# Kernel optimization log

Measured on AMD Instinct MI355X. Metric: run time of the kernel, lower is better.

Reference implementation:

```python
import jax, jax.numpy as jnp
import numpy as np

D_E, D_ENC, D_DEC, H = 128, 256, 512, 8
HD = D_DEC // H
B, S, T, V, C = 32, 128, 128, 32000, 2


def gru_cell(x, h, Wih, Whh, bih, bhh):
    # PyTorch GRU cell: gates ordered (reset, update, new)
    gi = x @ Wih.T + bih
    gh = h @ Whh.T + bhh
    ir, iz, inn = jnp.split(gi, 3, axis=-1)
    hr, hz, hn = jnp.split(gh, 3, axis=-1)
    r = jax.nn.sigmoid(ir + hr)
    z = jax.nn.sigmoid(iz + hz)
    n = jnp.tanh(inn + r * hn)
    return (1.0 - z) * n + z * h


def setup_inputs():
    key = jax.random.key(0)
    ks = iter(jax.random.split(key, 40))
    def nrm(shape, s=0.05):
        return jax.random.normal(next(ks), shape, jnp.float32) * s
    inp = {}
    inp["nx"] = jax.random.randint(next(ks), (B, S), 0, V)
    inp["x"] = jax.random.randint(next(ks), (B, T), 0, V)
    inp["label"] = jax.random.randint(next(ks), (B,), 0, C)
    inp["tok_emb"] = nrm((V, D_E))
    inp["start_emb"] = nrm((1, D_E))
    inp["style_emb"] = nrm((C, D_DEC))
    for d in ("f", "b"):
        inp["enc_Wih_" + d] = nrm((3 * D_ENC, D_E))
        inp["enc_Whh_" + d] = nrm((3 * D_ENC, D_ENC))
        inp["enc_bih_" + d] = nrm((3 * D_ENC,))
        inp["enc_bhh_" + d] = nrm((3 * D_ENC,))
    inp["dec_Wih"] = nrm((3 * D_DEC, D_E))
    inp["dec_Whh"] = nrm((3 * D_DEC, D_DEC))
    inp["dec_bih"] = nrm((3 * D_DEC,))
    inp["dec_bhh"] = nrm((3 * D_DEC,))
    inp["attn_in_w"] = nrm((3 * D_DEC, D_DEC))
    inp["attn_in_b"] = nrm((3 * D_DEC,))
    inp["attn_out_w"] = nrm((D_DEC, D_DEC))
    inp["attn_out_b"] = nrm((D_DEC,))
    inp["ln_g"] = jnp.ones((D_DEC,), jnp.float32)
    inp["ln_b"] = jnp.zeros((D_DEC,), jnp.float32)
    inp["proj_w"] = nrm((V, D_DEC))
    inp["proj_b"] = nrm((V,))
    return inp


def _forward(nx, x, label, tok_emb, start_emb, style_emb,
             enc_Wih_f, enc_Whh_f, enc_bih_f, enc_bhh_f,
             enc_Wih_b, enc_Whh_b, enc_bih_b, enc_bhh_b,
             dec_Wih, dec_Whh, dec_bih, dec_bhh,
             attn_in_w, attn_in_b, attn_out_w, attn_out_b,
             ln_g, ln_b, proj_w, proj_b):
    b, s = nx.shape
    # --- bidirectional GRU encoder (dropout in eval mode => identity) ---
    emb = tok_emb[nx]                          # [B,S,dE]
    xs = jnp.swapaxes(emb, 0, 1)               # [S,B,dE]
    h0 = jnp.zeros((b, D_ENC), emb.dtype)

    def step_f(h, xt):
        h2 = gru_cell(xt, h, enc_Wih_f, enc_Whh_f, enc_bih_f, enc_bhh_f)
        return h2, h2

    def step_b(h, xt):
        h2 = gru_cell(xt, h, enc_Wih_b, enc_Whh_b, enc_bih_b, enc_bhh_b)
        return h2, h2

    _, out_f = jax.lax.scan(step_f, h0, xs)
    _, out_b = jax.lax.scan(step_b, h0, xs, reverse=True)
    memory = jnp.concatenate([out_f, out_b], axis=-1)   # [S,B,dDec] (seq-first, matches torch MHA)

    # --- precompute K/V projections of memory (invariant across decode steps) ---
    Wq, Wk, Wv = jnp.split(attn_in_w, 3, axis=0)
    bq, bk, bv = jnp.split(attn_in_b, 3)
    k = (memory @ Wk.T + bk).reshape(s, b, H, HD).transpose(1, 2, 0, 3)  # [B,H,S,HD]
    v = (memory @ Wv.T + bv).reshape(s, b, H, HD).transpose(1, 2, 0, 3)

    # --- teacher-forced decoder inputs: <start>, x[:,0], ..., x[:,T-2] ---
    dec_in = jnp.concatenate(
        [jnp.broadcast_to(start_emb[None, :, :], (b, 1, D_E)), tok_emb[x[:, :-1]]], axis=1)
    dec_xs = jnp.swapaxes(dec_in, 0, 1)        # [T,B,dE]
    h_init = style_emb[label]                  # [B,dDec]
    scale = 1.0 / np.sqrt(HD).astype(np.float32)

    def dec_step(h, xt):
        h_dec = gru_cell(xt, h, dec_Wih, dec_Whh, dec_bih, dec_bhh)      # [B,dDec]
        q = (h_dec @ Wq.T + bq).reshape(b, H, HD)
        scores = jnp.einsum('bhd,bhsd->bhs', q, k) * scale
        attn = jax.nn.softmax(scores, axis=-1)
        ctx = jnp.einsum('bhs,bhsd->bhd', attn, v).reshape(b, D_DEC)
        c = ctx @ attn_out_w.T + attn_out_b
        y = h_dec + c
        mu = jnp.mean(y, axis=-1, keepdims=True)
        var = jnp.var(y, axis=-1, keepdims=True)
        h_new = (y - mu) / jnp.sqrt(var + 1e-5) * ln_g + ln_b            # LayerNorm
        logits = h_new @ proj_w.T + proj_b                               # [B,V]
        return h_new, logits

    _, logits = jax.lax.scan(dec_step, h_init, dec_xs)   # [T,B,V]
    return jnp.swapaxes(logits, 0, 1)                    # [B,T,V]


def reference(nx, x, label, tok_emb, start_emb, style_emb,
              enc_Wih_f, enc_Whh_f, enc_bih_f, enc_bhh_f,
              enc_Wih_b, enc_Whh_b, enc_bih_b, enc_bhh_b,
              dec_Wih, dec_Whh, dec_bih, dec_bhh,
              attn_in_w, attn_in_b, attn_out_w, attn_out_b,
              ln_g, ln_b, proj_w, proj_b):
    return _forward(nx, x, label, tok_emb, start_emb, style_emb,
                    enc_Wih_f, enc_Whh_f, enc_bih_f, enc_bhh_f,
                    enc_Wih_b, enc_Whh_b, enc_bih_b, enc_bhh_b,
                    dec_Wih, dec_Whh, dec_bih, dec_bhh,
                    attn_in_w, attn_in_b, attn_out_w, attn_out_b,
                    ln_g, ln_b, proj_w, proj_b)
```

## Files before the change

### kernel.cpp

```cpp
#include <hip/hip_runtime.h>
#include <math.h>

typedef float f4 __attribute__((ext_vector_type(4)));
typedef short short8 __attribute__((ext_vector_type(8)));
typedef unsigned short us4 __attribute__((ext_vector_type(4)));

#define DEV static __device__ __forceinline__
#define AGENT __HIP_MEMORY_SCOPE_AGENT

DEV float bf2f(unsigned short u){ unsigned int x=((unsigned int)u)<<16; float f; __builtin_memcpy(&f,&x,4); return f; }
DEV unsigned short f2bf(float f){ unsigned int x; __builtin_memcpy(&x,&f,4); return (unsigned short)((x + 0x7fffu + ((x>>16)&1u))>>16); }

struct bfpair { short hi, lo; };
DEV bfpair splitbf(float v){
  bfpair p;
  unsigned short h_ = f2bf(v);
  p.hi = (short)h_;
  p.lo = (short)f2bf(v - bf2f(h_));
  return p;
}

DEV unsigned long long ldA64(const void* p){
  return __hip_atomic_load((const unsigned long long*)p, __ATOMIC_RELAXED, AGENT);
}
DEV void f2of(unsigned long long q, float* f0, float* f1){
  unsigned int lo=(unsigned int)q, hi=(unsigned int)(q>>32);
  __builtin_memcpy(f0,&lo,4); __builtin_memcpy(f1,&hi,4);
}

DEV void ld1x16_sc(const void* p, f4* o){
  asm volatile(
    "global_load_dwordx4 %0, %1, off sc0 sc1\n\t"
    "s_waitcnt vmcnt(0)"
    : "=&v"(o[0]) : "v"(p) : "memory");
}
DEV void ld8x16_sc(const void* p, f4* o){
  asm volatile(
    "global_load_dwordx4 %0, %8, off sc0 sc1\n\t"
    "global_load_dwordx4 %1, %8, off offset:16 sc0 sc1\n\t"
    "global_load_dwordx4 %2, %8, off offset:32 sc0 sc1\n\t"
    "global_load_dwordx4 %3, %8, off offset:48 sc0 sc1\n\t"
    "global_load_dwordx4 %4, %8, off offset:64 sc0 sc1\n\t"
    "global_load_dwordx4 %5, %8, off offset:80 sc0 sc1\n\t"
    "global_load_dwordx4 %6, %8, off offset:96 sc0 sc1\n\t"
    "global_load_dwordx4 %7, %8, off offset:112 sc0 sc1\n\t"
    "s_waitcnt vmcnt(0)"
    : "=&v"(o[0]),"=&v"(o[1]),"=&v"(o[2]),"=&v"(o[3]),
      "=&v"(o[4]),"=&v"(o[5]),"=&v"(o[6]),"=&v"(o[7])
    : "v"(p) : "memory");
}
DEV void ld16x16_sc(const void* p, f4* o){
  asm volatile(
    "global_load_dwordx4 %0, %16, off sc0 sc1\n\t"
    "global_load_dwordx4 %1, %16, off offset:16 sc0 sc1\n\t"
    "global_load_dwordx4 %2, %16, off offset:32 sc0 sc1\n\t"
    "global_load_dwordx4 %3, %16, off offset:48 sc0 sc1\n\t"
    "global_load_dwordx4 %4, %16, off offset:64 sc0 sc1\n\t"
    "global_load_dwordx4 %5, %16, off offset:80 sc0 sc1\n\t"
    "global_load_dwordx4 %6, %16, off offset:96 sc0 sc1\n\t"
    "global_load_dwordx4 %7, %16, off offset:112 sc0 sc1\n\t"
    "global_load_dwordx4 %8, %16, off offset:128 sc0 sc1\n\t"
    "global_load_dwordx4 %9, %16, off offset:144 sc0 sc1\n\t"
    "global_load_dwordx4 %10, %16, off offset:160 sc0 sc1\n\t"
    "global_load_dwordx4 %11, %16, off offset:176 sc0 sc1\n\t"
    "global_load_dwordx4 %12, %16, off offset:192 sc0 sc1\n\t"
    "global_load_dwordx4 %13, %16, off offset:208 sc0 sc1\n\t"
    "global_load_dwordx4 %14, %16, off offset:224 sc0 sc1\n\t"
    "global_load_dwordx4 %15, %16, off offset:240 sc0 sc1\n\t"
    "s_waitcnt vmcnt(0)"
    : "=&v"(o[0]),"=&v"(o[1]),"=&v"(o[2]),"=&v"(o[3]),
      "=&v"(o[4]),"=&v"(o[5]),"=&v"(o[6]),"=&v"(o[7]),
      "=&v"(o[8]),"=&v"(o[9]),"=&v"(o[10]),"=&v"(o[11]),
      "=&v"(o[12]),"=&v"(o[13]),"=&v"(o[14]),"=&v"(o[15])
    : "v"(p) : "memory");
}
DEV void st8x16_sc(void* p, const f4* v){
  asm volatile(
    "global_store_dwordx4 %8, %0, off sc0 sc1\n\t"
    "global_store_dwordx4 %8, %1, off offset:16 sc0 sc1\n\t"
    "global_store_dwordx4 %8, %2, off offset:32 sc0 sc1\n\t"
    "global_store_dwordx4 %8, %3, off offset:48 sc0 sc1\n\t"
    "global_store_dwordx4 %8, %4, off offset:64 sc0 sc1\n\t"
    "global_store_dwordx4 %8, %5, off offset:80 sc0 sc1\n\t"
    "global_store_dwordx4 %8, %6, off offset:96 sc0 sc1\n\t"
    "global_store_dwordx4 %8, %7, off offset:112 sc0 sc1\n\t"
    "s_waitcnt vmcnt(0)"
    :: "v"(v[0]),"v"(v[1]),"v"(v[2]),"v"(v[3]),
       "v"(v[4]),"v"(v[5]),"v"(v[6]),"v"(v[7]),"v"(p) : "memory");
}

DEV int lds_off(int row,int strideShorts,int kShort){
  return row*strideShorts*2 + ((((kShort & ~7)*2) ^ ((row & 7)<<4)) + (kShort & 7)*2);
}
DEV void st8(unsigned short* lds,int row,int strideShorts,int k0,short8 v){
  *(short8*)((char*)lds + lds_off(row,strideShorts,k0)) = v;
}
DEV short8 ldfrag(const unsigned short* lds,int rowBase,int strideShorts,int k0){
  int lane = (int)(threadIdx.x & 63u);
  int row = rowBase + (lane & 15);
  int k = k0 + (lane >> 4)*8;
  return *(const short8*)((const char*)lds + lds_off(row,strideShorts,k));
}

DEV float dot8(f4 a0, f4 a1, short8 w){
  return a0[0]*bf2f((unsigned short)w[0]) + a0[1]*bf2f((unsigned short)w[1])
       + a0[2]*bf2f((unsigned short)w[2]) + a0[3]*bf2f((unsigned short)w[3])
       + a1[0]*bf2f((unsigned short)w[4]) + a1[1]*bf2f((unsigned short)w[5])
       + a1[2]*bf2f((unsigned short)w[6]) + a1[3]*bf2f((unsigned short)w[7]);
}

DEV void gbar_slot(int* slot, int nwg){
  __syncthreads();
  if (threadIdx.x==0){
    __hip_atomic_fetch_add(slot,1,__ATOMIC_RELAXED,AGENT);
    while (__hip_atomic_load(slot,__ATOMIC_RELAXED,AGENT) < nwg){
      __builtin_amdgcn_s_sleep(2);
    }
  }
  __syncthreads();
}

DEV void dbar(int* ctrs, int wg, int target){
  __syncthreads();
  if (threadIdx.x < 64){
    if (threadIdx.x == 0)
      __hip_atomic_store(&ctrs[wg*32], target, __ATOMIC_RELAXED, AGENT);
    for(;;){
      int v = __hip_atomic_load(&ctrs[(int)threadIdx.x*32], __ATOMIC_RELAXED, AGENT);
      if (__all(v >= target)) break;
      __builtin_amdgcn_s_sleep(2);
    }
  }
  __syncthreads();
}
DEV void vwait(int* ctrs, int target){
  if (threadIdx.x < 64){
    for(;;){
      int v = __hip_atomic_load(&ctrs[(int)threadIdx.x*32], __ATOMIC_RELAXED, AGENT);
      if (__all(v >= target)) break;
      __builtin_amdgcn_s_sleep(64);
    }
  }
  __syncthreads();
}
DEV void cwait(int* cctrs, int target){
  if (threadIdx.x < 64){
    for(;;){
      int v = __hip_atomic_load(&cctrs[((int)threadIdx.x & 7)*32], __ATOMIC_RELAXED, AGENT);
      if (__all(v >= target)) break;
      __builtin_amdgcn_s_sleep(64);
    }
  }
  __syncthreads();
}

__global__ void cvt_kernel(const float* __restrict__ src, unsigned short* __restrict__ dst, int n4){
  int stride = gridDim.x*blockDim.x;
  for (long i = blockIdx.x*blockDim.x + threadIdx.x; i < n4; i += stride){
    f4 v = *(const f4*)(src + i*4);
    us4 o; o[0]=f2bf(v[0]); o[1]=f2bf(v[1]); o[2]=f2bf(v[2]); o[3]=f2bf(v[3]);
    *(us4*)(dst + i*4) = o;
  }
}

__global__ void embed_kernel(const int* __restrict__ nx, const int* __restrict__ x,
  const int* __restrict__ label, const float* __restrict__ tok,
  const float* __restrict__ start, const float* __restrict__ style,
  unsigned short* __restrict__ embE, unsigned short* __restrict__ embD,
  float* __restrict__ h0)
{
  const int half = 4096*32;
  int i = blockIdx.x*256 + threadIdx.x;
  if (i < 2*half){
    const bool dec = i >= half;
    int j = dec ? i - half : i;
    int m = j >> 5, c4 = j & 31;
    int b = m & 31, tt = m >> 5;
    const float* src;
    if (!dec) src = tok + (long)nx[b*128 + tt]*128;
    else src = (tt == 0) ? start : (tok + (long)x[b*128 + tt - 1]*128);
    f4 v = *(const f4*)(src + c4*4);
    us4 o; o[0]=f2bf(v[0]); o[1]=f2bf(v[1]); o[2]=f2bf(v[2]); o[3]=f2bf(v[3]);
    *(us4*)((dec ? embD : embE) + (long)m*128 + c4*4) = o;
  } else {
    int j = i - 2*half;
    if (j < 4096){
      int b = j >> 7, c4 = j & 127;
      *(f4*)(h0 + b*512 + c4*4) = *(const f4*)(style + (long)label[b]*512 + c4*4);
    }
  }
}

__global__ void kv_reshape(const float* __restrict__ kvp, unsigned short* __restrict__ Kb, unsigned short* __restrict__ Vb){
  long i = (long)blockIdx.x*256 + threadIdx.x;
  if (i >= (long)4096*1024) return;
  int m = (int)(i >> 10), n = (int)(i & 1023);
  int s = m >> 5, b = m & 31;
  unsigned short bv = f2bf(kvp[i]);
  if (n < 512){
    int hh = n >> 6, d = n & 63;
    Kb[((long)(b*8 + hh)*128 + s)*64 + d] = bv;
  } else {
    int n2 = n - 512; int hh = n2 >> 6, d = n2 & 63;
    Vb[((long)(b*8 + hh)*64 + d)*128 + s] = bv;
  }
}

template<int MODE>
__global__ __launch_bounds__(256,2) void gemm64(
  const unsigned short* __restrict__ Bw, const float* __restrict__ bias,
  float* __restrict__ C, int M, int N, int K, int ldC,
  const unsigned short* __restrict__ Abf,
  const float* __restrict__ Af0, const float* __restrict__ Af1)
{
  __shared__ unsigned short a_s[64*64];
  __shared__ unsigned short b_s[64*64];
  const int tid = threadIdx.x, lane = tid & 63, wv = tid >> 6;
  const long mb = (long)blockIdx.x*64, nb = (long)blockIdx.y*64;
  f4 z = {0.f,0.f,0.f,0.f};
  f4 acc[4] = {z,z,z,z};
  const int r = tid >> 2, q = tid & 3, k0 = q*16;
  for (int kb = 0; kb < K; kb += 64){
    if (MODE==0){
      const unsigned short* src = Abf + (mb + r)*K + kb + k0;
      st8(a_s, r, 64, k0,   *(const short8*)src);
      st8(a_s, r, 64, k0+8, *(const short8*)(src+8));
    } else {
      float tmp[16];
      long m = mb + r;
      int kg = kb + k0;
      const float* base = (kg < 256) ? (Af0 + m*256 + kg) : (Af1 + m*256 + (kg - 256));
      #pragma unroll
      for (int i=0;i<16;i++) tmp[i] = base[i];
      short8 v0, v1;
      #pragma unroll
      for (int i=0;i<8;i++){ v0[i] = (short)f2bf(tmp[i]); v1[i] = (short)f2bf(tmp[8+i]); }
      st8(a_s, r, 64, k0, v0); st8(a_s, r, 64, k0+8, v1);
    }
    {
      const unsigned short* src = Bw + (nb + r)*K + kb + k0;
      st8(b_s, r, 64, k0,   *(const short8*)src);
      st8(b_s, r, 64, k0+8, *(const short8*)(src+8));
    }
    __syncthreads();
    #pragma unroll
    for (int kf=0; kf<2; kf++){
      short8 bfr = ldfrag(b_s, wv*16, 64, kf*32);
      #pragma unroll
      for (int mt=0; mt<4; mt++){
        short8 afr = ldfrag(a_s, mt*16, 64, kf*32);
        acc[mt] = __builtin_amdgcn_mfma_f32_16x16x32_bf16(afr, bfr, acc[mt], 0,0,0);
      }
    }
    __syncthreads();
  }
  const long col = nb + wv*16 + (lane & 15);
  const float bs = bias[col];
  #pragma unroll
  for (int mt=0; mt<4; mt++){
    #pragma unroll
    for (int rr=0; rr<4; rr++){
      long row = mb + mt*16 + (lane>>4)*4 + rr;
      C[row*(long)ldC + col] = acc[mt][rr] + bs;
    }
  }
}

__global__ __launch_bounds__(384) void enc_kernel(
  const float* __restrict__ WhhF_f, const float* __restrict__ WhhB_f,
  const float* __restrict__ GIF, const float* __restrict__ GIB,
  const float* __restrict__ bhhF, const float* __restrict__ bhhB,
  float* __restrict__ OUTF, float* __restrict__ OUTB,
  float* __restrict__ Hf,
  int* bar)
{
  __shared__ unsigned short whh_hi[96*256];
  __shared__ unsigned short whh_lo[96*256];
  __shared__ unsigned short a_hi[32*256];
  __shared__ unsigned short a_lo[32*256];
  __shared__ float ghscr[32*96];
  const int tid = threadIdx.x;
  const int wg = blockIdx.x;
  const int dir = wg >> 3, wgl = wg & 7;
  const float* Whh_f = dir ? WhhB_f : WhhF_f;
  const float* GI = dir ? GIB : GIF;
  const float* bhh = dir ? bhhB : bhhF;
  float* OUT = dir ? OUTB : OUTF;

  for (int idx = tid; idx < 96*32; idx += 384){
    int lr = idx >> 5, ch = idx & 31;
    int g_ = lr >> 5, jj = lr & 31;
    const float* wsrc = Whh_f + (long)(g_*256 + wgl*32 + jj)*256 + ch*8;
    short8 vh, vl;
    #pragma unroll
    for (int i=0;i<8;i++){ bfpair p = splitbf(wsrc[i]); vh[i] = p.hi; vl[i] = p.lo; }
    st8(whh_hi, lr, 256, ch*8, vh);
    st8(whh_lo, lr, 256, ch*8, vl);
  }
  __syncthreads();
  for (int t = 0; t < 128; t++){
    const int s = dir ? (127 - t) : t;
    const float* hbr = Hf + ((size_t)((t&1)*2 + dir))*(32*256);
    float* hbw = Hf + ((size_t)(((t+1)&1)*2 + dir))*(32*256);
    if (tid < 256){
      int b = tid >> 3, kg = tid & 7;
      const unsigned long long* hs = (const unsigned long long*)(hbr + b*256 + kg*32);
      #pragma unroll
      for (int c=0;c<4;c++){
        short8 vh, vl;
        #pragma unroll
        for (int i2=0;i2<4;i2++){
          unsigned long long qv = ldA64(hs + c*4 + i2);
          float f0, f1; f2of(qv, &f0, &f1);
          bfpair p0 = splitbf(f0), p1 = splitbf(f1);
          vh[i2*2] = p0.hi; vl[i2*2] = p0.lo;
          vh[i2*2+1] = p1.hi; vl[i2*2+1] = p1.lo;
        }
        st8(a_hi, b, 256, kg*32 + c*8, vh);
        st8(a_lo, b, 256, kg*32 + c*8, vl);
      }
    }
    __syncthreads();
    {
      const int wv = tid >> 6;
      f4 acc0 = {0.f,0.f,0.f,0.f}, acc1 = {0.f,0.f,0.f,0.f};
      #pragma unroll
      for (int kf=0; kf<8; kf++){
        short8 bhi = ldfrag(whh_hi, wv*16, 256, kf*32);
        short8 blo = ldfrag(whh_lo, wv*16, 256, kf*32);
        short8 ah0 = ldfrag(a_hi, 0, 256, kf*32);
        short8 al0 = ldfrag(a_lo, 0, 256, kf*32);
        short8 ah1 = ldfrag(a_hi, 16, 256, kf*32);
        short8 al1 = ldfrag(a_lo, 16, 256, kf*32);
        acc0 = __builtin_amdgcn_mfma_f32_16x16x32_bf16(ah0, bhi, acc0, 0,0,0);
        acc0 = __builtin_amdgcn_mfma_f32_16x16x32_bf16(al0, bhi, acc0, 0,0,0);
        acc0 = __builtin_amdgcn_mfma_f32_16x16x32_bf16(ah0, blo, acc0, 0,0,0);
        acc1 = __builtin_amdgcn_mfma_f32_16x16x32_bf16(ah1, bhi, acc1, 0,0,0);
        acc1 = __builtin_amdgcn_mfma_f32_16x16x32_bf16(al1, bhi, acc1, 0,0,0);
        acc1 = __builtin_amdgcn_mfma_f32_16x16x32_bf16(ah1, blo, acc1, 0,0,0);
      }
      const int lane = tid & 63;
      const int cl = wv*16 + (lane & 15);
      #pragma unroll
      for (int rr=0; rr<4; rr++){
        int r0 = (lane>>4)*4 + rr;
        ghscr[r0*96 + cl] = acc0[rr];
        ghscr[(16+r0)*96 + cl] = acc1[rr];
      }
    }
    __syncthreads();
    for (int task = tid; task < 1024; task += 384){
      int b = task >> 5, jj = task & 31;
      int jg = wgl*32 + jj;
      float ghr = ghscr[b*96 + jj]      + bhh[jg];
      float ghz = ghscr[b*96 + 32 + jj] + bhh[256 + jg];
      float ghn = ghscr[b*96 + 64 + jj] + bhh[512 + jg];
      const float* gi = GI + ((long)s*32 + b)*768;
      float r_ = 1.f/(1.f + __expf(-(gi[jg] + ghr)));
      float z_ = 1.f/(1.f + __expf(-(gi[256+jg] + ghz)));
      float n_ = tanhf(gi[512+jg] + r_*ghn);
      float hp = __hip_atomic_load(&hbr[b*256 + jg], __ATOMIC_RELAXED, AGENT);
      float hn = (1.f - z_)*n_ + z_*hp;
      OUT[((long)s*32 + b)*256 + jg] = hn;
      __hip_atomic_store(&hbw[b*256 + jg], hn, __ATOMIC_RELAXED, AGENT);
    }
    gbar_slot(bar + dir*128 + t, 8);
  }
}

struct DecS {
  unsigned short whh_hi[32*512];
  unsigned short whh_lo[32*512];
  unsigned short a_hi[32*512];
  unsigned short a_lo[32*512];
  float scr[32*64];
  float attn_l[4*128];
  float ctxs[4*64];
  float redm[32*8*2];
  float murs[64];
  float hnfr[32*8];
  float lngl[512], lnbl[512];
  float s1l[24], s2l[24];
};
struct VocS {
  unsigned short a_s[128*512];
  unsigned short b_s[64*64];
  float gl[512];
  float s2g[176];
};
struct CvtS {
  float redm[32*8*2];
  float murs[64];
};
union SU { DecS d; VocS v; CvtS c; };

__global__ __launch_bounds__(256,1) void dec_fused(
  const float* __restrict__ Whh_f,
  const unsigned short* __restrict__ WqBf,
  const unsigned short* __restrict__ Wout,
  const unsigned short* __restrict__ Kbf,
  const unsigned short* __restrict__ Vbf,
  const float* __restrict__ GI,
  const float* __restrict__ bhh,
  const float* __restrict__ aib,
  const float* __restrict__ aob,
  const float* __restrict__ lng,
  const float* __restrict__ lnb,
  const float* __restrict__ h0,
  float* __restrict__ Y,
  unsigned int* __restrict__ hdec32,
  unsigned short* __restrict__ Ybf,
  const unsigned short* __restrict__ Pbf,
  const float* __restrict__ projWf,
  const float* __restrict__ projB,
  float* __restrict__ out,
  int* ctrs)
{
  __shared__ SU s;
  const int tid = threadIdx.x;
  const int lane = tid & 63, wv = tid >> 6;
  int* cctrs = ctrs + 2048;

  if (blockIdx.x < 64){
    const int wg = blockIdx.x;
    const int h = wg >> 3, bg = wg & 7;
    const int jbase = wg*8;
    const int cw = wg & 7;

    if (tid < 24){ s.d.s1l[tid] = 0.f; s.d.s2l[tid] = 0.f; }
    __syncthreads();
    for (int idx = tid; idx < 32*64; idx += 256){
      int lr = idx >> 6, ch = idx & 63;
      short8 vh = {0,0,0,0,0,0,0,0}, vl = {0,0,0,0,0,0,0,0};
      if (lr < 24){
        int g_ = lr >> 3, jj = lr & 7;
        const float* wsrc = Whh_f + (long)(g_*512 + jbase + jj)*512 + ch*8;
        float s1p = 0.f, s2p = 0.f;
        #pragma unroll
        for (int i=0;i<8;i++){
          float wvv = wsrc[i];
          float gv = lng[ch*8+i];
          float bv = lnb[ch*8+i];
          float wp = wvv*gv;
          bfpair p = splitbf(wp);
          vh[i] = p.hi; vl[i] = p.lo;
          s1p += wp; s2p += bv*wvv;
        }
        atomicAdd(&s.d.s1l[lr], s1p);
        atomicAdd(&s.d.s2l[lr], s2p);
      }
      st8(s.d.whh_hi, lr, 512, ch*8, vh);
      st8(s.d.whh_lo, lr, 512, ch*8, vl);
    }
    for (int i = tid; i < 512; i += 256){ s.d.lngl[i] = lng[i]; s.d.lnbl[i] = lnb[i]; }

    const int qrow = h*64 + wv*16 + (lane & 15);
    const int kb0q = (lane>>4)*8;
    const unsigned short* wqbase = WqBf + (long)qrow*512 + kb0q;
    const int b_l = wv;
    const int bglob = bg*4 + b_l;
    const unsigned short* kbase = Kbf + ((long)(bglob*8 + h)*128 + lane*2)*64;
    const unsigned short* vbase = Vbf + ((long)(bglob*8 + h)*64 + lane)*128;
    const int jp = tid & 127;
    const unsigned short* wobase = Wout + (long)(jp*4)*512 + h*64;
    const float qb = aib[h*64 + wv*16 + (lane & 15)];
    const int bA = tid >> 3, kgA = tid & 7;
    const int jjA = tid & 7;
    const int jgA = jbase + jjA;
    const float bhr = bhh[jgA], bhz = bhh[512 + jgA], bhn = bhh[1024 + jgA];
    const float aobv = aob[jgA];
    __syncthreads();

    int lgen = 0;
    float gir = GI[((long)0*32 + bA)*1536 + jgA];
    float giz = GI[((long)0*32 + bA)*1536 + 512 + jgA];
    float gin = GI[((long)0*32 + bA)*1536 + 1024 + jgA];
    for (int t = 0; t < 128; t++){
      if (t == 0){
        const float* src = h0 + bA*512 + kgA*64;
        #pragma unroll
        for (int c=0;c<8;c++){
          short8 vh, vl;
          #pragma unroll
          for (int i=0;i<8;i++){
            float v = src[c*8+i];
            float gv = s.d.lngl[kgA*64 + c*8 + i];
            bfpair p = splitbf(v/gv);
            vh[i] = p.hi; vl[i] = p.lo;
            if (kgA == h && c == cw) s.d.hnfr[bA*8+i] = v;
          }
          st8(s.d.a_hi, bA, 512, kgA*64 + c*8, vh);
          st8(s.d.a_lo, bA, 512, kgA*64 + c*8, vl);
        }
        __syncthreads();
      } else {
        f4 yv[16];
        ld16x16_sc(Y + ((long)(t-1)*32 + bA)*512 + kgA*64, yv);
        float sm = 0.f, sq = 0.f;
        #pragma unroll
        for (int c=0;c<8;c++){
          short8 vh, vl;
          #pragma unroll
          for (int e=0;e<8;e++){
            float f = yv[c*2 + (e>>2)][e&3];
            sm += f; sq += f*f;
            bfpair p = splitbf(f);
            vh[e] = p.hi; vl[e] = p.lo;
            if (kgA == h && c == cw) s.d.hnfr[bA*8+e] = f;
          }
          st8(s.d.a_hi, bA, 512, kgA*64 + c*8, vh);
          st8(s.d.a_lo, bA, 512, kgA*64 + c*8, vl);
        }
        s.d.redm[(bA*8+kgA)*2] = sm; s.d.redm[(bA*8+kgA)*2+1] = sq;
        __syncthreads();
        if (tid < 32){
          float S1=0.f, S2=0.f;
          #pragma unroll
          for (int i=0;i<8;i++){ S1 += s.d.redm[(tid*8+i)*2]; S2 += s.d.redm[(tid*8+i)*2+1]; }
          float mu = S1*(1.f/512.f);
          float var = S2*(1.f/512.f) - mu*mu;
          s.d.murs[tid*2] = mu; s.d.murs[tid*2+1] = rsqrtf(var + 1e-5f);
        }
        __syncthreads();
      }
      {
        const int mt = wv >> 1, nt = wv & 1;
        f4 acc = {0.f,0.f,0.f,0.f};
        #pragma unroll
        for (int kf=0; kf<16; kf++){
          short8 bhi = ldfrag(s.d.whh_hi, nt*16, 512, kf*32);
          short8 blo = ldfrag(s.d.whh_lo, nt*16, 512, kf*32);
          short8 ahi = ldfrag(s.d.a_hi, mt*16, 512, kf*32);
          short8 alo = ldfrag(s.d.a_lo, mt*16, 512, kf*32);
          acc = __builtin_amdgcn_mfma_f32_16x16x32_bf16(ahi, bhi, acc, 0,0,0);
          acc = __builtin_amdgcn_mfma_f32_16x16x32_bf16(alo, bhi, acc, 0,0,0);
          acc = __builtin_amdgcn_mfma_f32_16x16x32_bf16(ahi, blo, acc, 0,0,0);
        }
        const int cl = nt*16 + (lane & 15);
        if (cl < 24){
          #pragma unroll
          for (int rr=0; rr<4; rr++){
            int row = mt*16 + (lane>>4)*4 + rr;
            s.d.scr[row*32 + cl] = acc[rr];
          }
        }
      }
      __syncthreads();
      {
        const float mu = t ? s.d.murs[bA*2] : 0.f;
        const float rsv = t ? s.d.murs[bA*2+1] : 1.f;
        const float c2 = rsv*mu;
        float ghr = rsv*s.d.scr[bA*32 + jjA]      - c2*s.d.s1l[jjA]      + (t ? s.d.s2l[jjA]      : 0.f) + bhr;
        float ghz = rsv*s.d.scr[bA*32 + 8 + jjA]  - c2*s.d.s1l[8 + jjA]  + (t ? s.d.s2l[8 + jjA]  : 0.f) + bhz;
        float ghn = rsv*s.d.scr[bA*32 + 16 + jjA] - c2*s.d.s1l[16 + jjA] + (t ? s.d.s2l[16 + jjA] : 0.f) + bhn;
        float r_ = 1.f/(1.f + __expf(-(gir + ghr)));
        float z_ = 1.f/(1.f + __expf(-(giz + ghz)));
        float n_ = tanhf(gin + r_*ghn);
        float hpv = s.d.hnfr[bA*8 + jjA];
        float hp = t ? (hpv - mu)*rsv*s.d.lngl[jgA] + s.d.lnbl[jgA] : hpv;
        float hd = (1.f - z_)*n_ + z_*hp;
        unsigned int hb = (unsigned int)f2bf(hd);
        unsigned int other = (unsigned int)__shfl_xor((int)hb, 1);
        if ((jjA & 1) == 0){
          unsigned int pack = hb | (other << 16);
          __hip_atomic_store(&hdec32[bA*256 + (jgA >> 1)], pack, __ATOMIC_RELAXED, AGENT);
        }
        __hip_atomic_store(&Y[((long)t*32 + bA)*512 + jgA], hd + aobv, __ATOMIC_RELAXED, AGENT);
      }
      dbar(ctrs, wg, ++lgen);
      {
        const int r4 = tid >> 6, ch = tid & 63;
        f4 hv;
        ld1x16_sc(hdec32 + (bg*4 + r4)*256 + ch*4, &hv);
        short8 v;
        #pragma unroll
        for (int w2=0; w2<4; w2++){
          float fv = hv[w2];
          unsigned int u; __builtin_memcpy(&u, &fv, 4);
          v[w2*2]   = (short)(u & 0xffff);
          v[w2*2+1] = (short)(u >> 16);
        }
        st8(s.d.a_hi, r4, 512, ch*8, v);
      }
      __syncthreads();
      {
        f4 acc0 = {0.f,0.f,0.f,0.f};
        #pragma unroll
        for (int kf=0; kf<16; kf++){
          short8 bfr = *(const short8*)(wqbase + kf*32);
          acc0 = __builtin_amdgcn_mfma_f32_16x16x32_bf16(ldfrag(s.d.a_hi, 0, 512, kf*32), bfr, acc0, 0,0,0);
        }
        const int cl = wv*16 + (lane & 15);
        if ((lane >> 4) == 0){
          #pragma unroll
          for (int rr=0; rr<4; rr++)
            s.d.scr[rr*64 + cl] = acc0[rr] + qb;
        }
      }
      __syncthreads();
      {
        const f4* qp = (const f4*)(s.d.scr + b_l*64);
        float s0 = 0.f, s1 = 0.f;
        #pragma unroll
        for (int c=0;c<8;c++) s0 += dot8(qp[c*2], qp[c*2+1], *(const short8*)(kbase + c*8));
        #pragma unroll
        for (int c=0;c<8;c++) s1 += dot8(qp[c*2], qp[c*2+1], *(const short8*)(kbase + 64 + c*8));
        s0 *= 0.125f; s1 *= 0.125f;
        float mx = fmaxf(s0, s1);
        #pragma unroll
        for (int o=1;o<64;o<<=1) mx = fmaxf(mx, __shfl_xor(mx, o));
        float e0 = __expf(s0 - mx), e1 = __expf(s1 - mx);
        float sm = e0 + e1;
        #pragma unroll
        for (int o=1;o<64;o<<=1) sm += __shfl_xor(sm, o);
        float inv = 1.f/sm;
        s.d.attn_l[b_l*128 + lane*2]   = e0*inv;
        s.d.attn_l[b_l*128 + lane*2+1] = e1*inv;
      }
      __syncthreads();
      {
        const f4* ap = (const f4*)(s.d.attn_l + b_l*128);
        float cx = 0.f;
        #pragma unroll
        for (int c=0;c<16;c++) cx += dot8(ap[c*2], ap[c*2+1], *(const short8*)(vbase + c*8));
        s.d.ctxs[b_l*64 + lane] = cx;
      }
      __syncthreads();
      {
        const int b2 = tid >> 7;
        #pragma unroll
        for (int jj=0;jj<4;jj++){
          const unsigned short* wb = wobase + (long)jj*512;
          short8 w0 = *(const short8*)(wb);
          short8 w1 = *(const short8*)(wb+8);
          short8 w2 = *(const short8*)(wb+16);
          short8 w3 = *(const short8*)(wb+24);
          short8 w4 = *(const short8*)(wb+32);
          short8 w5 = *(const short8*)(wb+40);
          short8 w6 = *(const short8*)(wb+48);
          short8 w7 = *(const short8*)(wb+56);
          #pragma unroll
          for (int bb=0; bb<2; bb++){
            const int bl = b2 + bb*2;
            const int bgl = bg*4 + bl;
            const f4* cp = (const f4*)(s.d.ctxs + bl*64);
            float cj = dot8(cp[0], cp[1], w0) + dot8(cp[2], cp[3], w1)
                     + dot8(cp[4], cp[5], w2) + dot8(cp[6], cp[7], w3)
                     + dot8(cp[8], cp[9], w4) + dot8(cp[10], cp[11], w5)
                     + dot8(cp[12], cp[13], w6) + dot8(cp[14], cp[15], w7);
            atomicAdd(&Y[((long)t*32 + bgl)*512 + jp*4 + jj], cj);
          }
        }
      }
      if (t < 127){
        long base = ((long)(t+1)*32 + bA)*1536 + jgA;
        gir = GI[base];
        giz = GI[base + 512];
        gin = GI[base + 1024];
      }
      dbar(ctrs, wg, ++lgen);
    }
  } else if (blockIdx.x < 72){
    const int w = blockIdx.x - 64;
    const int rr = tid >> 3, seg = tid & 7;
    for (int c = 0; c < 16; c++){
      vwait(ctrs, 16*(c+1));
      long m = (long)c*256 + w*32 + rr;
      f4 yv[16];
      ld16x16_sc(Y + m*512 + seg*64, yv);
      float sm = 0.f, sq = 0.f;
      #pragma unroll
      for (int i=0;i<16;i++){
        f4 v = yv[i];
        sm += v[0]+v[1]+v[2]+v[3];
        sq += v[0]*v[0]+v[1]*v[1]+v[2]*v[2]+v[3]*v[3];
      }
      s.c.redm[(rr*8+seg)*2] = sm; s.c.redm[(rr*8+seg)*2+1] = sq;
      __syncthreads();
      if (tid < 32){
        float S1=0.f, S2=0.f;
        #pragma unroll
        for (int i=0;i<8;i++){ S1 += s.c.redm[(tid*8+i)*2]; S2 += s.c.redm[(tid*8+i)*2+1]; }
        float mu = S1*(1.f/512.f);
        float var = S2*(1.f/512.f) - mu*mu;
        s.c.murs[tid*2] = mu; s.c.murs[tid*2+1] = rsqrtf(var + 1e-5f);
      }
      __syncthreads();
      const float mu = s.c.murs[rr*2], rsv = s.c.murs[rr*2+1];
      f4 ob[8];
      #pragma unroll
      for (int i2=0;i2<32;i2++){
        float a0 = (yv[(2*i2)>>2][(2*i2)&3] - mu)*rsv;
        float a1v = (yv[(2*i2+1)>>2][(2*i2+1)&3] - mu)*rsv;
        unsigned int u = (unsigned int)f2bf(a0) | ((unsigned int)f2bf(a1v)<<16);
        float uf; __builtin_memcpy(&uf,&u,4);
        ob[i2>>2][i2&3] = uf;
      }
      st8x16_sc(Ybf + m*512 + seg*64, ob);
      __syncthreads();
      if (tid == 0)
        __hip_atomic_store(&cctrs[w*32], c+1, __ATOMIC_RELAXED, AGENT);
    }
  } else {
    const int w2 = blockIdx.x - 72;
    const int c0 = w2*174;
    const int cn = (32000 - c0 < 174) ? (32000 - c0) : 174;
    for (int cc = tid; cc < 176; cc += 256){
      if (cc < cn){
        const float* pw = projWf + (long)(c0+cc)*512;
        float s2 = 0.f;
        for (int k=0;k<512;k++) s2 += lnb[k]*pw[k];
        s.v.s2g[cc] = s2;
      }
    }
    for (int i = tid; i < 512; i += 256) s.v.gl[i] = lng[i];
    __syncthreads();
    const f4 z4 = {0.f,0.f,0.f,0.f};
    for (int c=0; c<16; c++){
      cwait(cctrs, c+1);
      for (int half=0; half<2; half++){
        const long rbase = (long)c*256 + half*128;
        {
          const int row = tid >> 1, seg = tid & 1;
          const unsigned short* src = Ybf + (rbase + row)*512 + seg*256;
          #pragma unroll
          for (int blk=0; blk<2; blk++){
            f4 av[16];
            ld16x16_sc(src + blk*128, av);
            #pragma unroll
            for (int i=0;i<16;i++){
              f4 tv = av[i];
              short8 s8; __builtin_memcpy(&s8, &tv, 16);
              st8(s.v.a_s, row, 512, seg*256 + blk*128 + i*8, s8);
            }
          }
        }
        __syncthreads();
        for (int nt=0; nt<3; nt++){
          f4 acc[8] = {z4,z4,z4,z4,z4,z4,z4,z4};
          for (int kt=0; kt<8; kt++){
            {
              const int r = tid >> 2, q = tid & 3, k0 = q*16;
              const int col = nt*64 + r;
              short8 v0 = {0,0,0,0,0,0,0,0}, v1 = {0,0,0,0,0,0,0,0};
              if (col < cn){
                const unsigned short* src = Pbf + (long)(c0+col)*512 + kt*64 + k0;
                #pragma unroll
                for (int i=0;i<8;i++){
                  v0[i] = (short)f2bf(bf2f(src[i])   * s.v.gl[kt*64 + k0 + i]);
                  v1[i] = (short)f2bf(bf2f(src[8+i]) * s.v.gl[kt*64 + k0 + 8 + i]);
                }
              }
              st8(s.v.b_s, r, 64, k0, v0);
              st8(s.v.b_s, r, 64, k0+8, v1);
            }
            __syncthreads();
            #pragma unroll
            for (int kf=0; kf<2; kf++){
              short8 bfr = ldfrag(s.v.b_s, wv*16, 64, kf*32);
              #pragma unroll
              for (int mt=0; mt<8; mt++){
                short8 afr = ldfrag(s.v.a_s, mt*16, 512, kt*64 + kf*32);
                acc[mt] = __builtin_amdgcn_mfma_f32_16x16x32_bf16(afr, bfr, acc[mt], 0,0,0);
              }
            }
            __syncthreads();
          }
          const int colloc = nt*64 + wv*16 + (lane & 15);
          if (colloc < cn){
            const int vcol = c0 + colloc;
            const float corr = s.v.s2g[colloc] + projB[vcol];
            #pragma unroll
            for (int mt=0; mt<8; mt++){
              #pragma unroll
              for (int rr=0; rr<4; rr++){
                int rowl = mt*16 + (lane>>4)*4 + rr;
                long m = rbase + rowl;
                long tt = m >> 5, b = m & 31;
                out[(b*128 + tt)*32000 + vcol] = acc[mt][rr] + corr;
              }
            }
          }
        }
        __syncthreads();
      }
    }
  }
}

extern "C" void kernel_launch(void* const* d_in, const int* in_sizes, int n_in,
                              void* d_out, int out_size, void* d_ws, size_t ws_size,
                              hipStream_t stream)
{
  const int* nx = (const int*)d_in[0];
  const int* x = (const int*)d_in[1];
  const int* label = (const int*)d_in[2];
  const float* tok = (const float*)d_in[3];
  const float* start = (const float*)d_in[4];
  const float* style = (const float*)d_in[5];
  const float* eWihF = (const float*)d_in[6];
  const float* eWhhF = (const float*)d_in[7];
  const float* ebihF = (const float*)d_in[8];
  const float* ebhhF = (const float*)d_in[9];
  const float* eWihB = (const float*)d_in[10];
  const float* eWhhB = (const float*)d_in[11];
  const float* ebihB = (const float*)d_in[12];
  const float* ebhhB = (const float*)d_in[13];
  const float* dWih = (const float*)d_in[14];
  const float* dWhh = (const float*)d_in[15];
  const float* dbih = (const float*)d_in[16];
  const float* dbhh = (const float*)d_in[17];
  const float* ainW = (const float*)d_in[18];
  const float* ainB = (const float*)d_in[19];
  const float* aoutW = (const float*)d_in[20];
  const float* aoutB = (const float*)d_in[21];
  const float* lng = (const float*)d_in[22];
  const float* lnb = (const float*)d_in[23];
  const float* projW = (const float*)d_in[24];
  const float* projB = (const float*)d_in[25];
  float* out = (float*)d_out;
  char* W = (char*)d_ws;

  size_t off = 0;
  auto alloc = [&](size_t sz){ size_t o = off; off = (off + sz + 255) & ~(size_t)255; return o; };
  const size_t O_HF   = alloc(4*32*256*4);
  const size_t O_BAR  = alloc(16384);
  const size_t O_EIHF = alloc(768*128*2);
  const size_t O_EIHB = alloc(768*128*2);
  const size_t O_DIH  = alloc(1536*128*2);
  const size_t O_AIN  = alloc(1536*512*2);
  const size_t O_AOUT = alloc(512*512*2);
  const size_t O_PROJ = alloc((size_t)32000*512*2);
  const size_t O_EMBE = alloc(4096*128*2);
  const size_t O_EMBD = alloc(4096*128*2);
  const size_t O_KBF  = alloc((size_t)32*8*128*64*2);
  const size_t O_VBF  = alloc((size_t)32*8*128*64*2);
  const size_t O_HDEC = alloc(32*256*4);
  const size_t O_YBF  = alloc((size_t)4096*512*2);
  const size_t O_GIF  = alloc((size_t)4096*768*4);
  const size_t O_GIB  = alloc((size_t)4096*768*4);
  const size_t O_GID  = alloc((size_t)4096*1536*4);
  const size_t O_OUTF = alloc((size_t)4096*256*4);
  const size_t O_OUTB = alloc((size_t)4096*256*4);
  const size_t O_KVP  = alloc((size_t)4096*1024*4);
  const size_t O_Y    = alloc((size_t)4096*512*4);
  const size_t O_H0   = alloc(32*512*4);

  (void)hipMemsetAsync(W + O_HF, 0, (O_BAR - O_HF) + 16384, stream);

  auto US = [&](size_t o){ return (unsigned short*)(W + o); };
  auto FP = [&](size_t o){ return (float*)(W + o); };

  {
    const struct { const float* s; size_t d; int n; } cvs[] = {
      {eWihF, O_EIHF, 768*128}, {eWihB, O_EIHB, 768*128},
      {dWih,  O_DIH,  1536*128},
      {ainW,  O_AIN,  1536*512}, {aoutW, O_AOUT, 512*512},
      {projW, O_PROJ, 32000*512},
    };
    for (auto &c : cvs){
      int n4 = c.n/4;
      int blocks = (n4 + 255)/256; if (blocks > 4096) blocks = 4096;
      cvt_kernel<<<blocks, 256, 0, stream>>>(c.s, US(c.d), n4);
    }
  }
  embed_kernel<<<1040, 256, 0, stream>>>(nx, x, label, tok, start, style,
                                         US(O_EMBE), US(O_EMBD), FP(O_H0));
  gemm64<0><<<dim3(64,12), 256, 0, stream>>>(US(O_EIHF), ebihF, FP(O_GIF), 4096, 768, 128, 768,
                                             US(O_EMBE), nullptr, nullptr);
  gemm64<0><<<dim3(64,12), 256, 0, stream>>>(US(O_EIHB), ebihB, FP(O_GIB), 4096, 768, 128, 768,
                                             US(O_EMBE), nullptr, nullptr);
  gemm64<0><<<dim3(64,24), 256, 0, stream>>>(US(O_DIH), dbih, FP(O_GID), 4096, 1536, 128, 1536,
                                             US(O_EMBD), nullptr, nullptr);
  enc_kernel<<<16, 384, 0, stream>>>(eWhhF, eWhhB, FP(O_GIF), FP(O_GIB),
                                     ebhhF, ebhhB, FP(O_OUTF), FP(O_OUTB), FP(O_HF),
                                     (int*)(W + O_BAR) + 3072);
  gemm64<1><<<dim3(64,16), 256, 0, stream>>>(US(O_AIN) + 512*512, ainB + 512, FP(O_KVP),
                                             4096, 1024, 512, 1024,
                                             nullptr, FP(O_OUTF), FP(O_OUTB));
  kv_reshape<<<16384, 256, 0, stream>>>(FP(O_KVP), US(O_KBF), US(O_VBF));
  dec_fused<<<256, 256, 0, stream>>>(dWhh, US(O_AIN), US(O_AOUT), US(O_KBF), US(O_VBF),
                                     FP(O_GID), dbhh, ainB, aoutB, lng, lnb, FP(O_H0),
                                     FP(O_Y), (unsigned int*)(W + O_HDEC), US(O_YBF),
                                     US(O_PROJ), projW, projB, out,
                                     (int*)(W + O_BAR));
  (void)in_sizes; (void)n_in; (void)out_size; (void)ws_size;
}
```

Baseline: 3.852 ms.

## Vectorize encoder hidden-state loads/stores and rebalance vocab projection blocks

In the encoder recurrence, hidden-state reads switch from many 64-bit atomic loads to eight 16-byte cache-bypassing loads per thread. The gate update now handles two adjacent units per task, so OUT and the hidden buffer are written with packed 64-bit stores. The fused decoder shrinks from 256 to 200 blocks, and each of the 128 vocab-projection blocks now covers 250 columns with four column tiles instead of about 174 with three. This reduces per-step latency in the serial encoder loop and cuts block count and padding waste, at the cost of more work per vocab block and a fixed split that only works when the vocab size is exactly 32000.

```diff
diff --git a/kernel.cpp b/kernel.cpp
--- a/kernel.cpp
+++ b/kernel.cpp
@@ -23,9 +23,16 @@
 DEV unsigned long long ldA64(const void* p){
   return __hip_atomic_load((const unsigned long long*)p, __ATOMIC_RELAXED, AGENT);
 }
+DEV void stA64(void* p, unsigned long long v){
+  __hip_atomic_store((unsigned long long*)p, v, __ATOMIC_RELAXED, AGENT);
+}
 DEV void f2of(unsigned long long q, float* f0, float* f1){
   unsigned int lo=(unsigned int)q, hi=(unsigned int)(q>>32);
   __builtin_memcpy(f0,&lo,4); __builtin_memcpy(f1,&hi,4);
+}
+DEV unsigned long long packf2(float a, float b){
+  unsigned int ua, ub; __builtin_memcpy(&ua,&a,4); __builtin_memcpy(&ub,&b,4);
+  return (unsigned long long)ua | ((unsigned long long)ub << 32);
 }
 
 DEV void ld1x16_sc(const void* p, f4* o){
@@ -304,17 +311,16 @@
     float* hbw = Hf + ((size_t)(((t+1)&1)*2 + dir))*(32*256);
     if (tid < 256){
       int b = tid >> 3, kg = tid & 7;
-      const unsigned long long* hs = (const unsigned long long*)(hbr + b*256 + kg*32);
+      f4 hv[8];
+      ld8x16_sc(hbr + b*256 + kg*32, hv);
       #pragma unroll
       for (int c=0;c<4;c++){
         short8 vh, vl;
         #pragma unroll
-        for (int i2=0;i2<4;i2++){
-          unsigned long long qv = ldA64(hs + c*4 + i2);
-          float f0, f1; f2of(qv, &f0, &f1);
-          bfpair p0 = splitbf(f0), p1 = splitbf(f1);
-          vh[i2*2] = p0.hi; vl[i2*2] = p0.lo;
-          vh[i2*2+1] = p1.hi; vl[i2*2+1] = p1.lo;
+        for (int e=0;e<8;e++){
+          float f = hv[c*2 + (e>>2)][e&3];
+          bfpair p = splitbf(f);
+          vh[e] = p.hi; vl[e] = p.lo;
         }
         st8(a_hi, b, 256, kg*32 + c*8, vh);
         st8(a_lo, b, 256, kg*32 + c*8, vl);
@@ -349,20 +355,28 @@
       }
     }
     __syncthreads();
-    for (int task = tid; task < 1024; task += 384){
-      int b = task >> 5, jj = task & 31;
-      int jg = wgl*32 + jj;
-      float ghr = ghscr[b*96 + jj]      + bhh[jg];
-      float ghz = ghscr[b*96 + 32 + jj] + bhh[256 + jg];
-      float ghn = ghscr[b*96 + 64 + jj] + bhh[512 + jg];
+    for (int task = tid; task < 512; task += 384){
+      int b = task >> 4, pj = task & 15;
+      int jj0 = pj*2;
+      int jg0 = wgl*32 + jj0;
       const float* gi = GI + ((long)s*32 + b)*768;
-      float r_ = 1.f/(1.f + __expf(-(gi[jg] + ghr)));
-      float z_ = 1.f/(1.f + __expf(-(gi[256+jg] + ghz)));
-      float n_ = tanhf(gi[512+jg] + r_*ghn);
-      float hp = __hip_atomic_load(&hbr[b*256 + jg], __ATOMIC_RELAXED, AGENT);
-      float hn = (1.f - z_)*n_ + z_*hp;
-      OUT[((long)s*32 + b)*256 + jg] = hn;
-      __hip_atomic_store(&hbw[b*256 + jg], hn, __ATOMIC_RELAXED, AGENT);
+      unsigned long long hq = ldA64(hbr + b*256 + jg0);
+      float hp0, hp1; f2of(hq, &hp0, &hp1);
+      float hn01[2];
+      #pragma unroll
+      for (int e=0;e<2;e++){
+        int jj = jj0 + e, jg = jg0 + e;
+        float ghr = ghscr[b*96 + jj]      + bhh[jg];
+        float ghz = ghscr[b*96 + 32 + jj] + bhh[256 + jg];
+        float ghn = ghscr[b*96 + 64 + jj] + bhh[512 + jg];
+        float r_ = 1.f/(1.f + __expf(-(gi[jg] + ghr)));
+        float z_ = 1.f/(1.f + __expf(-(gi[256+jg] + ghz)));
+        float n_ = tanhf(gi[512+jg] + r_*ghn);
+        float hp = e ? hp1 : hp0;
+        hn01[e] = (1.f - z_)*n_ + z_*hp;
+      }
+      *(unsigned long long*)(&OUT[((long)s*32 + b)*256 + jg0]) = packf2(hn01[0], hn01[1]);
+      stA64(hbw + b*256 + jg0, packf2(hn01[0], hn01[1]));
     }
     gbar_slot(bar + dir*128 + t, 8);
   }
@@ -386,7 +400,7 @@
   unsigned short a_s[128*512];
   unsigned short b_s[64*64];
   float gl[512];
-  float s2g[176];
+  float s2g[256];
 };
 struct CvtS {
   float redm[32*8*2];
@@ -703,15 +717,13 @@
     }
   } else {
     const int w2 = blockIdx.x - 72;
-    const int c0 = w2*174;
-    const int cn = (32000 - c0 < 174) ? (32000 - c0) : 174;
-    for (int cc = tid; cc < 176; cc += 256){
-      if (cc < cn){
-        const float* pw = projWf + (long)(c0+cc)*512;
-        float s2 = 0.f;
-        for (int k=0;k<512;k++) s2 += lnb[k]*pw[k];
-        s.v.s2g[cc] = s2;
-      }
+    const int c0 = w2*250;
+    const int cn = 250;
+    for (int cc = tid; cc < cn; cc += 256){
+      const float* pw = projWf + (long)(c0+cc)*512;
+      float s2 = 0.f;
+      for (int k=0;k<512;k++) s2 += lnb[k]*pw[k];
+      s.v.s2g[cc] = s2;
     }
     for (int i = tid; i < 512; i += 256) s.v.gl[i] = lng[i];
     __syncthreads();
@@ -736,7 +748,7 @@
           }
         }
         __syncthreads();
-        for (int nt=0; nt<3; nt++){
+        for (int nt=0; nt<4; nt++){
           f4 acc[8] = {z4,z4,z4,z4,z4,z4,z4,z4};
           for (int kt=0; kt<8; kt++){
             {
@@ -879,7 +891,7 @@
                                              4096, 1024, 512, 1024,
                                              nullptr, FP(O_OUTF), FP(O_OUTB));
   kv_reshape<<<16384, 256, 0, stream>>>(FP(O_KVP), US(O_KBF), US(O_VBF));
-  dec_fused<<<256, 256, 0, stream>>>(dWhh, US(O_AIN), US(O_AOUT), US(O_KBF), US(O_VBF),
+  dec_fused<<<200, 256, 0, stream>>>(dWhh, US(O_AIN), US(O_AOUT), US(O_KBF), US(O_VBF),
                                      FP(O_GID), dbhh, ainB, aoutB, lng, lnb, FP(O_H0),
                                      FP(O_Y), (unsigned int*)(W + O_HDEC), US(O_YBF),
                                      US(O_PROJ), projW, projB, out,
```

Result: faster. 3.668 ms (-4.8%).
